# Kernel tuning notes

Hardware: AMD Instinct MI355X
Metric: run time of the kernel (lower is better)

The kernel has to match this reference:

```python
import jax, jax.numpy as jnp
import numpy as np
import math

EMBED_DIM = 768
NUM_HEADS = 12
HEAD_DIM = EMBED_DIM // NUM_HEADS
EPS = 1e-6


def setup_inputs() -> dict:
    key = jax.random.key(0)
    ks = jax.random.split(key, 9)
    T, B, N, D = 4, 4, 1024, EMBED_DIM
    s = 0.02
    return {
        "x": jax.random.normal(ks[0], (T, B, N, D), dtype=jnp.float32),
        "Wq": jax.random.normal(ks[1], (D, D), dtype=jnp.float32) * s,
        "bq": jax.random.normal(ks[2], (D,), dtype=jnp.float32) * s,
        "Wk": jax.random.normal(ks[3], (D, D), dtype=jnp.float32) * s,
        "bk": jax.random.normal(ks[4], (D,), dtype=jnp.float32) * s,
        "Wv": jax.random.normal(ks[5], (D, D), dtype=jnp.float32) * s,
        "bv": jax.random.normal(ks[6], (D,), dtype=jnp.float32) * s,
        "Wo": jax.random.normal(ks[7], (D, D), dtype=jnp.float32) * s,
        "bo": jax.random.normal(ks[8], (D,), dtype=jnp.float32) * s,
    }


def _split_heads(y, T, B, N):
    # [T,B,N,D] -> [T,B,H,N,Dh]
    return y.reshape(T, B, N, NUM_HEADS, HEAD_DIM).transpose(0, 1, 3, 2, 4)


def reference(x, Wq, bq, Wk, bk, Wv, bv, Wo, bo):
    T, B, N, D = x.shape
    # q/k/v projections (nn.Linear: x @ W^T + b)
    q = _split_heads(x @ Wq.T + bq, T, B, N)
    k = _split_heads(x @ Wk.T + bk, T, B, N)
    v = _split_heads(x @ Wv.T + bv, T, B, N)
    # scores = q k^T / sqrt(head_dim)
    scores = jnp.einsum("tbhnd,tbhmd->tbhnm", q, k) / math.sqrt(HEAD_DIM)
    # spike-form normalization: relu then L1-normalize along keys
    act = jax.nn.relu(scores)
    attn = act / (act.sum(axis=-1, keepdims=True) + EPS)
    ctx = jnp.einsum("tbhnm,tbhmd->tbhnd", attn, v)
    # merge heads: [T,B,H,N,Dh] -> [T,B,N,D]
    out = ctx.transpose(0, 1, 3, 2, 4).reshape(T, B, N, D)
    return out @ Wo.T + bo
```

## Files before the change

kernel.cpp:

```cpp
#include <hip/hip_runtime.h>
#include <hip/hip_bf16.h>
#include <cstdint>


typedef __attribute__((ext_vector_type(8))) short short8;
typedef __attribute__((ext_vector_type(4))) float float4v;
typedef __attribute__((ext_vector_type(16))) float float16v;

__device__ __forceinline__ unsigned short f2bf(float f) {
  unsigned int u = __float_as_uint(f);
  u = (u + 0x7fffu + ((u >> 16) & 1u)) >> 16;
  return (unsigned short)u;
}

__device__ __forceinline__ unsigned int pkbf(float a, float b) {
  unsigned int ua = __float_as_uint(a) + 0x8000u;
  unsigned int ub = __float_as_uint(b) + 0x8000u;
  return __builtin_amdgcn_perm(ub, ua, 0x07060302u);
}

__device__ __forceinline__ void gld_lds16(const void* g, void* lds) {
  __builtin_amdgcn_global_load_lds(
      (__attribute__((address_space(1))) void*)(uintptr_t)g,
      (__attribute__((address_space(3))) void*)(uint32_t)(uintptr_t)lds,
      16, 0, 0);
}

__global__ __launch_bounds__(256) void cast_all(
    const float* __restrict__ x,  const float* __restrict__ Wq,
    const float* __restrict__ Wk, const float* __restrict__ Wv,
    const float* __restrict__ Wo, unsigned short* __restrict__ XBF,
    unsigned short* __restrict__ WQKV, unsigned short* __restrict__ WOb) {
  const int bid = blockIdx.x;
  const float* src;
  unsigned short* dst;
  int i;
  if (bid < 12288) {
    src = x; dst = XBF; i = bid * 256 + threadIdx.x;
  } else {
    const int wb = bid - 12288;
    const int which = wb / 576;
    i = (wb % 576) * 256 + threadIdx.x;
    src = (which == 0) ? Wq : (which == 1) ? Wk : (which == 2) ? Wv : Wo;
    dst = (which == 0) ? WQKV
        : (which == 1) ? WQKV + 589824
        : (which == 2) ? WQKV + 1179648 : WOb;
  }
  float4 f = reinterpret_cast<const float4*>(src)[i];
  ushort4 o;
  o.x = f2bf(f.x); o.y = f2bf(f.y); o.z = f2bf(f.z); o.w = f2bf(f.w);
  reinterpret_cast<ushort4*>(dst)[i] = o;
}

template <bool OUT_BF16>
__global__ __launch_bounds__(256) void gemm_bt(
    const unsigned short* __restrict__ A,
    const unsigned short* __restrict__ Bt,
    unsigned short* __restrict__ Cb,
    float* __restrict__ Cf,
    unsigned short* __restrict__ Vt,
    const float* __restrict__ b0, const float* __restrict__ b1,
    const float* __restrict__ b2, int N) {
  constexpr int K = 768;
  __shared__ unsigned short As[2][128 * 32];
  __shared__ unsigned short Bs[2][128 * 32];

  const int tid = threadIdx.x;
  const int lane = tid & 63;
  const int w = tid >> 6;
  const int wrow = w >> 1, wcol = w & 1;
  const int l15 = lane & 15, quad = lane >> 4;

  const int gx = gridDim.x;
  const int nwg = gx * gridDim.y;
  const int hw = blockIdx.y * gx + blockIdx.x;
  const int per = nwg >> 3;
  const int lg = (hw & 7) * per + (hw >> 3);
  const int bx = lg % gx, by = lg / gx;
  const int i0 = by * 128, j0 = bx * 128;

  const unsigned short* ga = A + (size_t)(i0 + 32 * w + (lane >> 2)) * K + (lane & 3) * 8;
  const unsigned short* gb = Bt + (size_t)(j0 + 32 * w + (lane >> 2)) * K + (lane & 3) * 8;

  float4v acc[4][4];
#pragma unroll
  for (int a = 0; a < 4; ++a)
#pragma unroll
    for (int b = 0; b < 4; ++b) acc[a][b] = float4v{0.f, 0.f, 0.f, 0.f};

  gld_lds16(ga, &As[0][(32 * w) * 32]);
  gld_lds16(ga + 16 * K, &As[0][(32 * w + 16) * 32]);
  gld_lds16(gb, &Bs[0][(32 * w) * 32]);
  gld_lds16(gb + 16 * K, &Bs[0][(32 * w + 16) * 32]);
  __syncthreads();

#pragma unroll 1
  for (int kt = 0; kt < K / 32; ++kt) {
    const int cur = kt & 1;
    if (kt < K / 32 - 1) {
      const unsigned short* pa = ga + (kt + 1) * 32;
      const unsigned short* pb = gb + (kt + 1) * 32;
      gld_lds16(pa, &As[cur ^ 1][(32 * w) * 32]);
      gld_lds16(pa + 16 * K, &As[cur ^ 1][(32 * w + 16) * 32]);
      gld_lds16(pb, &Bs[cur ^ 1][(32 * w) * 32]);
      gld_lds16(pb + 16 * K, &Bs[cur ^ 1][(32 * w + 16) * 32]);
    }

    short8 af[4], bfr[4];
#pragma unroll
    for (int a = 0; a < 4; ++a)
      af[a] = *(const short8*)&As[cur][(wrow * 64 + a * 16 + l15) * 32 + quad * 8];
#pragma unroll
    for (int b = 0; b < 4; ++b)
      bfr[b] = *(const short8*)&Bs[cur][(wcol * 64 + b * 16 + l15) * 32 + quad * 8];
#pragma unroll
    for (int a = 0; a < 4; ++a)
#pragma unroll
      for (int b = 0; b < 4; ++b)
        acc[a][b] = __builtin_amdgcn_mfma_f32_16x16x32_bf16(af[a], bfr[b], acc[a][b], 0, 0, 0);
    __syncthreads();
  }

  const int sel = j0 / 768;
  const float* bp = (sel == 0) ? b0 : ((sel == 1) ? b1 : b2);
#pragma unroll
  for (int a = 0; a < 4; ++a) {
    const int row0 = i0 + wrow * 64 + a * 16 + quad * 4;
#pragma unroll
    for (int b = 0; b < 4; ++b) {
      const int col = j0 + wcol * 64 + b * 16 + l15;
      const float bias = bp[col - sel * 768];
      if (OUT_BF16 && sel == 2) {
        const int tb = row0 >> 10;
        const int n0 = row0 & 1023;
        const int hd = col - 1536;
        const float v0 = acc[a][b][0] + bias;
        const float v1 = acc[a][b][1] + bias;
        const float v2 = acc[a][b][2] + bias;
        const float v3 = acc[a][b][3] + bias;
        uint2 u;
        u.x = (unsigned int)f2bf(v0) | ((unsigned int)f2bf(v1) << 16);
        u.y = (unsigned int)f2bf(v2) | ((unsigned int)f2bf(v3) << 16);
        *(uint2*)&Vt[((size_t)(tb * 768 + hd)) * 1024 + n0] = u;
      } else {
#pragma unroll
        for (int r = 0; r < 4; ++r) {
          const float v = acc[a][b][r] + bias;
          if (OUT_BF16)
            Cb[(size_t)(row0 + r) * N + col] = f2bf(v);
          else
            Cf[(size_t)(row0 + r) * N + col] = v;
        }
      }
    }
  }
}

__global__ __launch_bounds__(256) void attn32(
    const unsigned short* __restrict__ qkv,
    const unsigned short* __restrict__ vt,
    unsigned short* __restrict__ ctx) {
  __shared__ unsigned short Ks[64 * 72];
  __shared__ unsigned short Vs[64 * 72];

  const int tbh = blockIdx.x;
  const int qt = blockIdx.y;
  const int tb = tbh / 12, h = tbh % 12;
  const int tid = threadIdx.x, lane = tid & 63, w = tid >> 6;
  const int l31 = lane & 31, hl = lane >> 5;

  short8 qf[2][4];
#pragma unroll
  for (int qs = 0; qs < 2; ++qs) {
    const unsigned short* qp =
        qkv + (size_t)(tb * 1024 + qt * 256 + w * 64 + qs * 32 + l31) * 2304 +
        h * 64 + hl * 8;
#pragma unroll
    for (int kc = 0; kc < 4; ++kc) qf[qs][kc] = *(const short8*)(qp + kc * 16);
  }

  const int srow = tid >> 3;
  const int sblk = tid & 7;
  const unsigned short* kcol =
      qkv + (size_t)(tb * 1024) * 2304 + 768 + h * 64 + sblk * 8;
  const unsigned short* vcol = vt + ((size_t)tbh * 64 + srow) * 1024 + sblk * 8;
  uint4 kr0, kr1, vr0, vr1;
  auto loadKV = [&](int kv) {
    const unsigned short* kp = kcol + (size_t)(kv * 64 + srow) * 2304;
    kr0 = *(const uint4*)kp;
    kr1 = *(const uint4*)(kp + 32 * 2304);
    const unsigned short* vp = vcol + kv * 64;
    vr0 = *(const uint4*)vp;
    vr1 = *(const uint4*)(vp + 32 * 1024);
  };

  float16v octx[2][2];
#pragma unroll
  for (int qs = 0; qs < 2; ++qs)
#pragma unroll
    for (int dt = 0; dt < 2; ++dt)
#pragma unroll
      for (int i = 0; i < 16; ++i) octx[qs][dt][i] = 0.f;
  float den[2] = {0.f, 0.f};

  loadKV(0);

#pragma unroll 1
  for (int kv = 0; kv < 16; ++kv) {
    __syncthreads();
    *(uint4*)&Ks[srow * 72 + sblk * 8] = kr0;
    *(uint4*)&Ks[(srow + 32) * 72 + sblk * 8] = kr1;
    *(uint4*)&Vs[srow * 72 + sblk * 8] = vr0;
    *(uint4*)&Vs[(srow + 32) * 72 + sblk * 8] = vr1;
    __syncthreads();
    if (kv < 15) loadKV(kv + 1);

#pragma unroll
    for (int qs = 0; qs < 2; ++qs) {
      unsigned int pk[2][8];
#pragma unroll
      for (int mt = 0; mt < 2; ++mt) {
        float16v st;
#pragma unroll
        for (int i = 0; i < 16; ++i) st[i] = 0.f;
#pragma unroll
        for (int kc = 0; kc < 4; ++kc) {
          short8 kf =
              *(const short8*)&Ks[(mt * 32 + l31) * 72 + kc * 16 + hl * 8];
          st = __builtin_amdgcn_mfma_f32_32x32x16_bf16(kf, qf[qs][kc], st, 0, 0, 0);
        }
#pragma unroll
        for (int g = 0; g < 4; ++g) {
          float v0 = st[4 * g + 0]; v0 = v0 > 0.f ? v0 : 0.f;
          float v1 = st[4 * g + 1]; v1 = v1 > 0.f ? v1 : 0.f;
          float v2 = st[4 * g + 2]; v2 = v2 > 0.f ? v2 : 0.f;
          float v3 = st[4 * g + 3]; v3 = v3 > 0.f ? v3 : 0.f;
          den[qs] += (v0 + v1) + (v2 + v3);
          pk[mt][g * 2 + 0] = pkbf(v0, v1);
          pk[mt][g * 2 + 1] = pkbf(v2, v3);
        }
      }
#pragma unroll
      for (int kc = 0; kc < 4; ++kc) {
        const int mt = kc >> 1, gb = (kc & 1) * 2;
        unsigned int a0 = pk[mt][gb * 2 + 0], b0 = pk[mt][gb * 2 + 2];
        unsigned int a1 = pk[mt][gb * 2 + 1], b1 = pk[mt][gb * 2 + 3];
        asm("v_permlane32_swap_b32 %0, %1" : "+v"(a0), "+v"(b0));
        asm("v_permlane32_swap_b32 %0, %1" : "+v"(a1), "+v"(b1));
        union { unsigned int u[4]; short8 s; } pf;
        pf.u[0] = a0; pf.u[1] = a1; pf.u[2] = b0; pf.u[3] = b1;
#pragma unroll
        for (int dt = 0; dt < 2; ++dt) {
          short8 vb =
              *(const short8*)&Vs[(dt * 32 + l31) * 72 + kc * 16 + hl * 8];
          octx[qs][dt] = __builtin_amdgcn_mfma_f32_32x32x16_bf16(
              vb, pf.s, octx[qs][dt], 0, 0, 0);
        }
      }
    }
  }

#pragma unroll
  for (int qs = 0; qs < 2; ++qs) {
    float d = den[qs] + __shfl_xor(den[qs], 32);
    const float sc = 1.f / (d + 8e-6f);
    const size_t qrow = (size_t)(tb * 1024 + qt * 256 + w * 64 + qs * 32 + l31);
#pragma unroll
    for (int dt = 0; dt < 2; ++dt)
#pragma unroll
      for (int g = 0; g < 4; ++g) {
        const float v0 = octx[qs][dt][4 * g + 0] * sc;
        const float v1 = octx[qs][dt][4 * g + 1] * sc;
        const float v2 = octx[qs][dt][4 * g + 2] * sc;
        const float v3 = octx[qs][dt][4 * g + 3] * sc;
        uint2 u;
        u.x = pkbf(v0, v1);
        u.y = pkbf(v2, v3);
        *(uint2*)&ctx[qrow * 768 + h * 64 + dt * 32 + g * 8 + hl * 4] = u;
      }
  }
}

extern "C" void kernel_launch(void* const* d_in, const int* in_sizes, int n_in,
                              void* d_out, int out_size, void* d_ws, size_t ws_size,
                              hipStream_t stream) {
  const float* x  = (const float*)d_in[0];
  const float* Wq = (const float*)d_in[1];
  const float* bq = (const float*)d_in[2];
  const float* Wk = (const float*)d_in[3];
  const float* bk = (const float*)d_in[4];
  const float* Wv = (const float*)d_in[5];
  const float* bv = (const float*)d_in[6];
  const float* Wo = (const float*)d_in[7];
  const float* bo = (const float*)d_in[8];
  float* out = (float*)d_out;

  char* ws = (char*)d_ws;
  unsigned short* XBF  = (unsigned short*)(ws);
  unsigned short* CTX  = (unsigned short*)(ws);
  unsigned short* WQKV = (unsigned short*)(ws + 25165824);
  unsigned short* WOb  = (unsigned short*)(ws + 28704768);
  unsigned short* QKV  = (unsigned short*)(ws + 29884416);
  unsigned short* VT   = (unsigned short*)(ws + 105381888);

  cast_all<<<14592, 256, 0, stream>>>(x, Wq, Wk, Wv, Wo, XBF, WQKV, WOb);

  gemm_bt<true><<<dim3(18, 128), 256, 0, stream>>>(XBF, WQKV, QKV, nullptr, VT,
                                                   bq, bk, bv, 2304);
  attn32<<<dim3(192, 4), 256, 0, stream>>>(QKV, VT, CTX);
  gemm_bt<false><<<dim3(6, 128), 256, 0, stream>>>(CTX, WOb, nullptr, out,
                                                   nullptr, bo, bo, bo, 768);
}
```

Baseline: 316.4 us.

## Triple-buffer GEMM LDS tiles with two-stage-ahead prefetch and partial vmcnt waits

Expands the projection GEMM's LDS staging from double to triple buffering and issues global-to-LDS loads two K-steps ahead. The full __syncthreads is replaced by a partial s_waitcnt vmcnt(4) plus a raw barrier, so only the oldest stage's loads must have landed before compute continues. The aim is to hide more global-memory latency behind the MFMA work. It costs 50% more LDS per block, which may lower occupancy, and it depends on the vmcnt counts exactly matching the number of loads issued per stage.

```diff
diff --git a/kernel.cpp b/kernel.cpp
--- a/kernel.cpp
+++ b/kernel.cpp
@@ -62,8 +62,9 @@
     const float* __restrict__ b0, const float* __restrict__ b1,
     const float* __restrict__ b2, int N) {
   constexpr int K = 768;
-  __shared__ unsigned short As[2][128 * 32];
-  __shared__ unsigned short Bs[2][128 * 32];
+  constexpr int KT = K / 32;
+  __shared__ unsigned short As[3][128 * 32];
+  __shared__ unsigned short Bs[3][128 * 32];
 
   const int tid = threadIdx.x;
   const int lane = tid & 63;
@@ -82,29 +83,31 @@
   const unsigned short* ga = A + (size_t)(i0 + 32 * w + (lane >> 2)) * K + (lane & 3) * 8;
   const unsigned short* gb = Bt + (size_t)(j0 + 32 * w + (lane >> 2)) * K + (lane & 3) * 8;
 
+  auto stage = [&](int kt2, int bufi) {
+    const unsigned short* pa = ga + kt2 * 32;
+    const unsigned short* pb = gb + kt2 * 32;
+    gld_lds16(pa, &As[bufi][(32 * w) * 32]);
+    gld_lds16(pa + 16 * K, &As[bufi][(32 * w + 16) * 32]);
+    gld_lds16(pb, &Bs[bufi][(32 * w) * 32]);
+    gld_lds16(pb + 16 * K, &Bs[bufi][(32 * w + 16) * 32]);
+  };
+
   float4v acc[4][4];
 #pragma unroll
   for (int a = 0; a < 4; ++a)
 #pragma unroll
     for (int b = 0; b < 4; ++b) acc[a][b] = float4v{0.f, 0.f, 0.f, 0.f};
 
-  gld_lds16(ga, &As[0][(32 * w) * 32]);
-  gld_lds16(ga + 16 * K, &As[0][(32 * w + 16) * 32]);
-  gld_lds16(gb, &Bs[0][(32 * w) * 32]);
-  gld_lds16(gb + 16 * K, &Bs[0][(32 * w + 16) * 32]);
-  __syncthreads();
+  stage(0, 0);
+  stage(1, 1);
+  asm volatile("s_waitcnt vmcnt(4)" ::: "memory");
+  __builtin_amdgcn_s_barrier();
+  __builtin_amdgcn_sched_barrier(0);
 
 #pragma unroll 1
-  for (int kt = 0; kt < K / 32; ++kt) {
-    const int cur = kt & 1;
-    if (kt < K / 32 - 1) {
-      const unsigned short* pa = ga + (kt + 1) * 32;
-      const unsigned short* pb = gb + (kt + 1) * 32;
-      gld_lds16(pa, &As[cur ^ 1][(32 * w) * 32]);
-      gld_lds16(pa + 16 * K, &As[cur ^ 1][(32 * w + 16) * 32]);
-      gld_lds16(pb, &Bs[cur ^ 1][(32 * w) * 32]);
-      gld_lds16(pb + 16 * K, &Bs[cur ^ 1][(32 * w + 16) * 32]);
-    }
+  for (int kt = 0; kt < KT; ++kt) {
+    const int cur = kt % 3;
+    if (kt + 2 < KT) stage(kt + 2, (kt + 2) % 3);
 
     short8 af[4], bfr[4];
 #pragma unroll
@@ -118,7 +121,16 @@
 #pragma unroll
       for (int b = 0; b < 4; ++b)
         acc[a][b] = __builtin_amdgcn_mfma_f32_16x16x32_bf16(af[a], bfr[b], acc[a][b], 0, 0, 0);
-    __syncthreads();
+
+    if (kt + 2 < KT) {
+      asm volatile("s_waitcnt vmcnt(4)" ::: "memory");
+      __builtin_amdgcn_s_barrier();
+      __builtin_amdgcn_sched_barrier(0);
+    } else if (kt + 1 < KT) {
+      asm volatile("s_waitcnt vmcnt(0)" ::: "memory");
+      __builtin_amdgcn_s_barrier();
+      __builtin_amdgcn_sched_barrier(0);
+    }
   }
 
   const int sel = j0 / 768;
```

After: 313.5 us. About the same (-0.9%).
